# Performance work log

Hardware: AMD Instinct MI355X
Metric: run time of the kernel (lower is better)

Reference implementation:

```python
import jax, jax.numpy as jnp
import numpy as np

N_NODES = 100000
N_EDGES = 600000
F_IN = 128
F_OUT = 128


def setup_inputs() -> dict:
    key = jax.random.key(0)
    ks = jax.random.split(key, 9)
    stdv = 1.0 / np.sqrt(F_OUT)
    return {
        "x": jax.random.normal(ks[0], (N_NODES, F_IN), dtype=jnp.float32),
        "weight": jax.random.uniform(ks[1], (F_IN, F_OUT), dtype=jnp.float32, minval=-stdv, maxval=stdv),
        "bias": jax.random.uniform(ks[2], (F_OUT,), dtype=jnp.float32, minval=-stdv, maxval=stdv),
        "vals0": jax.random.uniform(ks[3], (N_EDGES,), dtype=jnp.float32),
        "vals1": jax.random.uniform(ks[4], (N_EDGES,), dtype=jnp.float32),
        "rows0": jax.random.randint(ks[5], (N_EDGES,), 0, N_NODES, dtype=jnp.int32),
        "cols0": jax.random.randint(ks[6], (N_EDGES,), 0, N_NODES, dtype=jnp.int32),
        "rows1": jax.random.randint(ks[7], (N_EDGES,), 0, N_NODES, dtype=jnp.int32),
        "cols1": jax.random.randint(ks[8], (N_EDGES,), 0, N_NODES, dtype=jnp.int32),
    }


def _spmm(rows, cols, vals, dense, n):
    # COO sparse [n,n] @ dense [n,f]: gather source rows, scale, scatter-add to dest rows
    msgs = dense[cols] * vals[:, None]          # [E, f]
    return jax.ops.segment_sum(msgs, rows, num_segments=n)


def reference(x, weight, bias, vals0, vals1, rows0, cols0, rows1, cols1):
    n = x.shape[0]
    support = x @ weight                         # [N, F_OUT] dense GEMM
    out = _spmm(rows0, cols0, vals0, support, n) \
        + _spmm(rows1, cols1, vals1, support, n)
    return out + bias
```

## Files before the change

### kernel.cpp

```cpp
#include <hip/hip_runtime.h>


#define FDIM 128

typedef __attribute__((ext_vector_type(8))) short short8;
typedef __attribute__((ext_vector_type(4))) float floatx4;

__device__ __forceinline__ unsigned short f32_to_bf16(float f) {
    unsigned int u = __float_as_uint(f);
    unsigned int r = u + 0x7fffu + ((u >> 16) & 1u);
    return (unsigned short)(r >> 16);
}

__global__ __launch_bounds__(256) void wt_conv(const float* __restrict__ w,
                                               unsigned short* __restrict__ wt) {
    int idx = blockIdx.x * 256 + threadIdx.x;
    int nn = idx >> 7, k = idx & 127;
    wt[idx] = f32_to_bf16(w[(size_t)k * FDIM + nn]);
}

__global__ __launch_bounds__(256) void gemm_mfma(const float* __restrict__ x,
                                                 const unsigned short* __restrict__ wt,
                                                 unsigned short* __restrict__ support,
                                                 int n) {
    __shared__ __align__(16) short As[64][136];
    __shared__ __align__(16) short Bs[128][136];
    const int tid = threadIdx.x;
    const int m0 = blockIdx.x * 64;

    #pragma unroll
    for (int i = 0; i < 8; ++i) {
        int idx = tid + i * 256;
        int r = idx >> 5, c4 = idx & 31;
        float4 v = make_float4(0.f, 0.f, 0.f, 0.f);
        if (m0 + r < n) v = *(const float4*)(x + (size_t)(m0 + r) * FDIM + c4 * 4);
        short4 s;
        s.x = (short)f32_to_bf16(v.x); s.y = (short)f32_to_bf16(v.y);
        s.z = (short)f32_to_bf16(v.z); s.w = (short)f32_to_bf16(v.w);
        *(short4*)&As[r][c4 * 4] = s;
    }
    #pragma unroll
    for (int i = 0; i < 8; ++i) {
        int idx = tid + i * 256;
        int r = idx >> 4, c8 = idx & 15;
        short8 v = *(const short8*)(wt + (size_t)r * FDIM + c8 * 8);
        *(short8*)&Bs[r][c8 * 8] = v;
    }
    __syncthreads();

    const int wv = tid >> 6;
    const int lane = tid & 63;
    const int quad = lane >> 4;
    const int lr = lane & 15;

    floatx4 acc[8];
    #pragma unroll
    for (int nt = 0; nt < 8; ++nt) acc[nt] = (floatx4)0.f;

    #pragma unroll
    for (int ks = 0; ks < 4; ++ks) {
        short8 a = *(const short8*)&As[wv * 16 + lr][ks * 32 + quad * 8];
        #pragma unroll
        for (int nt = 0; nt < 8; ++nt) {
            short8 b = *(const short8*)&Bs[nt * 16 + lr][ks * 32 + quad * 8];
            acc[nt] = __builtin_amdgcn_mfma_f32_16x16x32_bf16(a, b, acc[nt], 0, 0, 0);
        }
    }

    #pragma unroll
    for (int i = 0; i < 4; ++i) {
        int row = m0 + wv * 16 + quad * 4 + i;
        if (row < n) {
            #pragma unroll
            for (int nt = 0; nt < 8; ++nt)
                support[(size_t)row * FDIM + nt * 16 + lr] = f32_to_bf16(acc[nt][i]);
        }
    }
}

__global__ __launch_bounds__(256) void build_rec(const int* __restrict__ rows0,
                                                 const int* __restrict__ cols0,
                                                 const float* __restrict__ vals0,
                                                 const int* __restrict__ rows1,
                                                 const int* __restrict__ cols1,
                                                 const float* __restrict__ vals1,
                                                 int* __restrict__ head,
                                                 int4* __restrict__ rec, int E) {
    int gid = blockIdx.x * 256 + threadIdx.x;
    if (gid >= 2 * E) return;
    int r, c; float v;
    if (gid < E) { r = rows0[gid]; c = cols0[gid]; v = vals0[gid]; }
    else         { int e = gid - E; r = rows1[e]; c = cols1[e]; v = vals1[e]; }
    int old = atomicExch(&head[r], gid);
    rec[gid] = make_int4(old, c, __float_as_int(v), 0);
}

__global__ __launch_bounds__(256) void pull_rec(const unsigned short* __restrict__ support,
                                                const int* __restrict__ head,
                                                const int4* __restrict__ rec,
                                                const float* __restrict__ bias,
                                                float* __restrict__ out, int n) {
    int wid = (blockIdx.x * 256 + threadIdx.x) >> 6;
    int lane = threadIdx.x & 63;
    if (wid >= n) return;
    float ax = 0.f, ay = 0.f;
    int e = head[wid];
    while (e >= 0) {
        int4 rc = rec[e];
        float v = __int_as_float(rc.z);
        unsigned int u = *(const unsigned int*)(support + (size_t)rc.y * FDIM + lane * 2);
        ax += v * __uint_as_float((u & 0xffffu) << 16);
        ay += v * __uint_as_float(u & 0xffff0000u);
        e = rc.x;
    }
    float2 b = *(const float2*)(bias + lane * 2);
    *(float2*)(out + (size_t)wid * FDIM + lane * 2) = make_float2(ax + b.x, ay + b.y);
}

__global__ __launch_bounds__(256) void init_bias(const float* __restrict__ bias,
                                                 float* __restrict__ out, int n) {
    int idx = blockIdx.x * 256 + threadIdx.x;
    int total = n * (FDIM / 4);
    if (idx < total) {
        int j = (idx & (FDIM / 4 - 1)) * 4;
        float4 b = *(const float4*)(bias + j);
        *(float4*)(out + (size_t)idx * 4) = b;
    }
}

__global__ __launch_bounds__(256) void scatter_bf16(
    const unsigned short* __restrict__ support,
    const int* __restrict__ rows0, const int* __restrict__ cols0, const float* __restrict__ vals0,
    const int* __restrict__ rows1, const int* __restrict__ cols1, const float* __restrict__ vals1,
    float* __restrict__ out, int E) {
    int gid = blockIdx.x * 256 + threadIdx.x;
    int lane = gid & 63;
    int eg = gid >> 6;
    if (eg >= 2 * E) return;
    int r, c; float v;
    if (eg < E) { r = rows0[eg]; c = cols0[eg]; v = vals0[eg]; }
    else        { int e = eg - E; r = rows1[e]; c = cols1[e]; v = vals1[e]; }
    unsigned int u = *(const unsigned int*)(support + (size_t)c * FDIM + lane * 2);
    float sx = __uint_as_float((u & 0xffffu) << 16);
    float sy = __uint_as_float(u & 0xffff0000u);
    float* op = out + (size_t)r * FDIM + lane * 2;
    atomicAdd(op,     sx * v);
    atomicAdd(op + 1, sy * v);
}

static inline size_t align256(size_t v) { return (v + 255) & ~(size_t)255; }

extern "C" void kernel_launch(void* const* d_in, const int* in_sizes, int n_in,
                              void* d_out, int out_size, void* d_ws, size_t ws_size,
                              hipStream_t stream) {
    const float* x     = (const float*)d_in[0];
    const float* w     = (const float*)d_in[1];
    const float* bias  = (const float*)d_in[2];
    const float* vals0 = (const float*)d_in[3];
    const float* vals1 = (const float*)d_in[4];
    const int*   rows0 = (const int*)d_in[5];
    const int*   cols0 = (const int*)d_in[6];
    const int*   rows1 = (const int*)d_in[7];
    const int*   cols1 = (const int*)d_in[8];
    const int n = in_sizes[0] / FDIM;
    const int E = in_sizes[3];
    float* out = (float*)d_out;

    size_t off = 0;
    unsigned short* support = (unsigned short*)((char*)d_ws + off);
    off = align256(off + (size_t)n * FDIM * 2);
    unsigned short* wt = (unsigned short*)((char*)d_ws + off);
    off = align256(off + (size_t)FDIM * FDIM * 2);
    int*  head = (int*)((char*)d_ws + off);   off = align256(off + (size_t)n * 4);
    int4* rec  = (int4*)((char*)d_ws + off);  off = align256(off + (size_t)2 * E * 16);

    wt_conv<<<(FDIM * FDIM) / 256, 256, 0, stream>>>(w, wt);
    gemm_mfma<<<(n + 63) / 64, 256, 0, stream>>>(x, wt, support, n);

    if (off <= ws_size) {
        hipMemsetAsync(head, 0xFF, (size_t)n * 4, stream);
        int eb = (2 * E + 255) / 256;
        build_rec<<<eb, 256, 0, stream>>>(rows0, cols0, vals0, rows1, cols1, vals1,
                                          head, rec, E);
        pull_rec<<<(n + 3) / 4, 256, 0, stream>>>(support, head, rec, bias, out, n);
    } else {
        int total4 = n * (FDIM / 4);
        init_bias<<<(total4 + 255) / 256, 256, 0, stream>>>(bias, out, n);
        long long tthreads = 2LL * E * 64;
        int blocks = (int)((tthreads + 255) / 256);
        scatter_bf16<<<blocks, 256, 0, stream>>>(support, rows0, cols0, vals0,
                                                 rows1, cols1, vals1, out, E);
    }
}
```

Before: 312.3 us.

## Replace linked-list edge chains with CSR built by histogram and scan

Replaces the atomicExch linked-list edge chains with a CSR layout. The layout is built by a row histogram, a three-kernel prefix scan and a cursor-based scatter of compact (col,val) records. The pull kernel then loads up to 64 edge records per wave at once, broadcasts them with shuffles, and issues four independent support-row gathers at a time. This removes the serial pointer-chasing latency of the old chain traversal, at the cost of four extra small kernel launches and a second atomic pass over the edges.

```diff
diff --git a/kernel.cpp b/kernel.cpp
--- a/kernel.cpp
+++ b/kernel.cpp
@@ -10,6 +10,13 @@
     unsigned int u = __float_as_uint(f);
     unsigned int r = u + 0x7fffu + ((u >> 16) & 1u);
     return (unsigned short)(r >> 16);
+}
+
+__device__ __forceinline__ float bf16_lo(unsigned int u) {
+    return __uint_as_float((u & 0xffffu) << 16);
+}
+__device__ __forceinline__ float bf16_hi(unsigned int u) {
+    return __uint_as_float(u & 0xffff0000u);
 }
 
 __global__ __launch_bounds__(256) void wt_conv(const float* __restrict__ w,
@@ -78,40 +85,143 @@
     }
 }
 
-__global__ __launch_bounds__(256) void build_rec(const int* __restrict__ rows0,
-                                                 const int* __restrict__ cols0,
-                                                 const float* __restrict__ vals0,
+__global__ __launch_bounds__(256) void hist_rows(const int* __restrict__ rows0,
                                                  const int* __restrict__ rows1,
-                                                 const int* __restrict__ cols1,
-                                                 const float* __restrict__ vals1,
-                                                 int* __restrict__ head,
-                                                 int4* __restrict__ rec, int E) {
+                                                 int* __restrict__ count, int E) {
+    int gid = blockIdx.x * 256 + threadIdx.x;
+    if (gid >= 2 * E) return;
+    int r = (gid < E) ? rows0[gid] : rows1[gid - E];
+    atomicAdd(&count[r], 1);
+}
+
+__device__ __forceinline__ int block_incl_scan(int v, int tid, int* lds) {
+    int lane = tid & 63, wv = tid >> 6;
+    #pragma unroll
+    for (int d = 1; d < 64; d <<= 1) {
+        int y = __shfl_up(v, d);
+        if (lane >= d) v += y;
+    }
+    if (lane == 63) lds[wv] = v;
+    __syncthreads();
+    if (wv == 0 && lane < 4) {
+        int s = lds[lane];
+        #pragma unroll
+        for (int d = 1; d < 4; d <<= 1) {
+            int y = __shfl_up(s, d);
+            if (lane >= d) s += y;
+        }
+        lds[4 + lane] = s;
+    }
+    __syncthreads();
+    int add = (wv > 0) ? lds[4 + wv - 1] : 0;
+    return v + add;
+}
+
+__global__ __launch_bounds__(256) void block_sum(const int* __restrict__ count,
+                                                 int* __restrict__ bsum, int n) {
+    __shared__ int lds[8];
+    int tid = threadIdx.x;
+    int idx = blockIdx.x * 256 + tid;
+    int v = (idx < n) ? count[idx] : 0;
+    int inc = block_incl_scan(v, tid, lds);
+    if (tid == 255) bsum[blockIdx.x] = inc;
+}
+
+__global__ __launch_bounds__(256) void scan_bsum(int* __restrict__ bsum, int nb) {
+    __shared__ int lds[8];
+    __shared__ int carry;
+    int tid = threadIdx.x;
+    if (tid == 0) carry = 0;
+    __syncthreads();
+    for (int base = 0; base < nb; base += 256) {
+        int i = base + tid;
+        int v = (i < nb) ? bsum[i] : 0;
+        int inc = block_incl_scan(v, tid, lds);
+        int c = carry;
+        if (i < nb) bsum[i] = c + inc - v;
+        __syncthreads();
+        if (tid == 255) carry = c + inc;
+        __syncthreads();
+    }
+}
+
+__global__ __launch_bounds__(256) void write_ptr(const int* __restrict__ count,
+                                                 const int* __restrict__ bscan,
+                                                 int* __restrict__ rowptr,
+                                                 int* __restrict__ cursor,
+                                                 int n, int total) {
+    __shared__ int lds[8];
+    int tid = threadIdx.x;
+    int idx = blockIdx.x * 256 + tid;
+    int v = (idx < n) ? count[idx] : 0;
+    int inc = block_incl_scan(v, tid, lds);
+    if (idx < n) {
+        int p = bscan[blockIdx.x] + inc - v;
+        rowptr[idx] = p;
+        cursor[idx] = p;
+    }
+    if (idx == 0) rowptr[n] = total;
+}
+
+__global__ __launch_bounds__(256) void scatter_rec(const int* __restrict__ rows0,
+                                                   const int* __restrict__ cols0,
+                                                   const float* __restrict__ vals0,
+                                                   const int* __restrict__ rows1,
+                                                   const int* __restrict__ cols1,
+                                                   const float* __restrict__ vals1,
+                                                   int* __restrict__ cursor,
+                                                   int2* __restrict__ rec, int E) {
     int gid = blockIdx.x * 256 + threadIdx.x;
     if (gid >= 2 * E) return;
     int r, c; float v;
     if (gid < E) { r = rows0[gid]; c = cols0[gid]; v = vals0[gid]; }
     else         { int e = gid - E; r = rows1[e]; c = cols1[e]; v = vals1[e]; }
-    int old = atomicExch(&head[r], gid);
-    rec[gid] = make_int4(old, c, __float_as_int(v), 0);
-}
-
-__global__ __launch_bounds__(256) void pull_rec(const unsigned short* __restrict__ support,
-                                                const int* __restrict__ head,
-                                                const int4* __restrict__ rec,
+    int pos = atomicAdd(&cursor[r], 1);
+    rec[pos] = make_int2(c, __float_as_int(v));
+}
+
+__global__ __launch_bounds__(256) void pull_csr(const unsigned short* __restrict__ support,
+                                                const int* __restrict__ rowptr,
+                                                const int2* __restrict__ rec,
                                                 const float* __restrict__ bias,
                                                 float* __restrict__ out, int n) {
     int wid = (blockIdx.x * 256 + threadIdx.x) >> 6;
     int lane = threadIdx.x & 63;
     if (wid >= n) return;
+    int beg = rowptr[wid], end = rowptr[wid + 1];
     float ax = 0.f, ay = 0.f;
-    int e = head[wid];
-    while (e >= 0) {
-        int4 rc = rec[e];
-        float v = __int_as_float(rc.z);
-        unsigned int u = *(const unsigned int*)(support + (size_t)rc.y * FDIM + lane * 2);
-        ax += v * __uint_as_float((u & 0xffffu) << 16);
-        ay += v * __uint_as_float(u & 0xffff0000u);
-        e = rc.x;
+    const char* sp = (const char*)support;
+    const unsigned loff = (unsigned)lane << 2;
+
+    for (int base = beg; base < end; base += 64) {
+        int m = end - base; if (m > 64) m = 64;
+        long long pk = 0;
+        if (lane < m) pk = *(const long long*)&rec[base + lane];
+        int j = 0;
+        for (; j + 4 <= m; j += 4) {
+            long long p0 = __shfl(pk, j);
+            long long p1 = __shfl(pk, j + 1);
+            long long p2 = __shfl(pk, j + 2);
+            long long p3 = __shfl(pk, j + 3);
+            unsigned u0 = *(const unsigned*)(sp + (((unsigned)p0) << 8) + loff);
+            unsigned u1 = *(const unsigned*)(sp + (((unsigned)p1) << 8) + loff);
+            unsigned u2 = *(const unsigned*)(sp + (((unsigned)p2) << 8) + loff);
+            unsigned u3 = *(const unsigned*)(sp + (((unsigned)p3) << 8) + loff);
+            float v0 = __int_as_float((int)(p0 >> 32));
+            float v1 = __int_as_float((int)(p1 >> 32));
+            float v2 = __int_as_float((int)(p2 >> 32));
+            float v3 = __int_as_float((int)(p3 >> 32));
+            ax += v0 * bf16_lo(u0); ay += v0 * bf16_hi(u0);
+            ax += v1 * bf16_lo(u1); ay += v1 * bf16_hi(u1);
+            ax += v2 * bf16_lo(u2); ay += v2 * bf16_hi(u2);
+            ax += v3 * bf16_lo(u3); ay += v3 * bf16_hi(u3);
+        }
+        for (; j < m; ++j) {
+            long long p = __shfl(pk, j);
+            unsigned u = *(const unsigned*)(sp + (((unsigned)p) << 8) + loff);
+            float v = __int_as_float((int)(p >> 32));
+            ax += v * bf16_lo(u); ay += v * bf16_hi(u);
+        }
     }
     float2 b = *(const float2*)(bias + lane * 2);
     *(float2*)(out + (size_t)wid * FDIM + lane * 2) = make_float2(ax + b.x, ay + b.y);
@@ -141,8 +251,8 @@
     if (eg < E) { r = rows0[eg]; c = cols0[eg]; v = vals0[eg]; }
     else        { int e = eg - E; r = rows1[e]; c = cols1[e]; v = vals1[e]; }
     unsigned int u = *(const unsigned int*)(support + (size_t)c * FDIM + lane * 2);
-    float sx = __uint_as_float((u & 0xffffu) << 16);
-    float sy = __uint_as_float(u & 0xffff0000u);
+    float sx = bf16_lo(u);
+    float sy = bf16_hi(u);
     float* op = out + (size_t)r * FDIM + lane * 2;
     atomicAdd(op,     sx * v);
     atomicAdd(op + 1, sy * v);
@@ -166,23 +276,32 @@
     const int E = in_sizes[3];
     float* out = (float*)d_out;
 
+    const int NB = (n + 255) / 256;
+
     size_t off = 0;
     unsigned short* support = (unsigned short*)((char*)d_ws + off);
     off = align256(off + (size_t)n * FDIM * 2);
     unsigned short* wt = (unsigned short*)((char*)d_ws + off);
     off = align256(off + (size_t)FDIM * FDIM * 2);
-    int*  head = (int*)((char*)d_ws + off);   off = align256(off + (size_t)n * 4);
-    int4* rec  = (int4*)((char*)d_ws + off);  off = align256(off + (size_t)2 * E * 16);
+    int*  count  = (int*)((char*)d_ws + off);  off = align256(off + (size_t)n * 4);
+    int*  rowptr = (int*)((char*)d_ws + off);  off = align256(off + (size_t)(n + 1) * 4);
+    int*  cursor = (int*)((char*)d_ws + off);  off = align256(off + (size_t)n * 4);
+    int*  bsum   = (int*)((char*)d_ws + off);  off = align256(off + (size_t)NB * 4);
+    int2* rec    = (int2*)((char*)d_ws + off); off = align256(off + (size_t)2 * E * 8);
 
     wt_conv<<<(FDIM * FDIM) / 256, 256, 0, stream>>>(w, wt);
     gemm_mfma<<<(n + 63) / 64, 256, 0, stream>>>(x, wt, support, n);
 
     if (off <= ws_size) {
-        hipMemsetAsync(head, 0xFF, (size_t)n * 4, stream);
+        hipMemsetAsync(count, 0, (size_t)n * 4, stream);
         int eb = (2 * E + 255) / 256;
-        build_rec<<<eb, 256, 0, stream>>>(rows0, cols0, vals0, rows1, cols1, vals1,
-                                          head, rec, E);
-        pull_rec<<<(n + 3) / 4, 256, 0, stream>>>(support, head, rec, bias, out, n);
+        hist_rows<<<eb, 256, 0, stream>>>(rows0, rows1, count, E);
+        block_sum<<<NB, 256, 0, stream>>>(count, bsum, n);
+        scan_bsum<<<1, 256, 0, stream>>>(bsum, NB);
+        write_ptr<<<NB, 256, 0, stream>>>(count, bsum, rowptr, cursor, n, 2 * E);
+        scatter_rec<<<eb, 256, 0, stream>>>(rows0, cols0, vals0, rows1, cols1, vals1,
+                                            cursor, rec, E);
+        pull_csr<<<(n + 3) / 4, 256, 0, stream>>>(support, rowptr, rec, bias, out, n);
     } else {
         int total4 = n * (FDIM / 4);
         init_bias<<<(total4 + 255) / 256, 256, 0, stream>>>(bias, out, n);
```

After: 325.8 us. 4.3% more time.
